# Performance work log

Measured on AMD Instinct MI355X. Metric: run time of the kernel, lower is better.

## Reference

```python
import jax, jax.numpy as jnp
import numpy as np

LN_EPS = 1e-5  # torch LayerNorm default
ITERS = 3

def _ln(x, g, b):
    m = jnp.mean(x, -1, keepdims=True)
    v = jnp.var(x, -1, keepdims=True)
    return (x - m) * jax.lax.rsqrt(v + LN_EPS) * g + b

def setup_inputs() -> dict:
    key = jax.random.key(0)
    ks = jax.random.split(key, 10)
    B, N, D, S, H = 32, 4096, 256, 8, 512
    sc = D ** -0.5
    w = lambda k, shape, s: jax.random.normal(k, shape, jnp.float32) * s
    return {
        "inputs": w(ks[0], (B, N, D), 1.0),
        "noise": w(ks[1], (B, S, D), 1.0),
        "ln_in_g": jnp.ones((D,), jnp.float32), "ln_in_b": jnp.zeros((D,), jnp.float32),
        "ln_slot_g": jnp.ones((D,), jnp.float32), "ln_slot_b": jnp.zeros((D,), jnp.float32),
        "ln_mlp_g": jnp.ones((D,), jnp.float32), "ln_mlp_b": jnp.zeros((D,), jnp.float32),
        "slot_mu": jnp.zeros((1, 1, D), jnp.float32),
        "slot_sigma": jnp.ones((1, 1, D), jnp.float32),
        "Wq": w(ks[2], (D, D), sc), "Wk": w(ks[3], (D, D), sc), "Wv": w(ks[4], (D, D), sc),
        "W_ih": w(ks[5], (D, 3 * D), sc), "W_hh": w(ks[6], (D, 3 * D), sc),
        "b_ih": jnp.zeros((3 * D,), jnp.float32), "b_hh": jnp.zeros((3 * D,), jnp.float32),
        "W1": w(ks[7], (D, H), sc), "b1": jnp.zeros((H,), jnp.float32),
        "W2": w(ks[8], (H, D), H ** -0.5), "b2": jnp.zeros((D,), jnp.float32),
    }

def reference(inputs, noise, ln_in_g, ln_in_b, ln_slot_g, ln_slot_b, ln_mlp_g, ln_mlp_b,
              slot_mu, slot_sigma, Wq, Wk, Wv, W_ih, W_hh, b_ih, b_hh, W1, b1, W2, b2):
    b, n, d = inputs.shape
    scale = d ** -0.5
    x = _ln(inputs, ln_in_g, ln_in_b)
    sigma = jnp.clip(jax.nn.softplus(slot_sigma), 0.1, 2.0)
    slots = slot_mu + sigma * noise            # [b, S, d]
    k = x @ Wk                                  # [b, n, d]
    v = x @ Wv                                  # [b, n, d]
    for _ in range(ITERS):
        slots_prev = slots
        s = _ln(slots, ln_slot_g, ln_slot_b)
        q = s @ Wq                              # [b, S, d]
        dots = jnp.einsum('bnd,bsd->bns', k, q) * scale
        attn = jax.nn.softmax(dots, axis=1)     # softmax over inputs (dim=1), as in source
        updates = jnp.einsum('bns,bnd->bsd', attn, v)
        # torch GRUCell: gate order (reset, update, new)
        gx = updates @ W_ih + b_ih
        gh = slots_prev @ W_hh + b_hh
        xr, xz, xn = jnp.split(gx, 3, -1)
        hr, hz, hn = jnp.split(gh, 3, -1)
        r = jax.nn.sigmoid(xr + hr)
        z = jax.nn.sigmoid(xz + hz)
        ng = jnp.tanh(xn + r * hn)
        slots = (1.0 - z) * ng + z * slots_prev
        m = _ln(slots, ln_mlp_g, ln_mlp_b)
        slots = slots + (jax.nn.relu(m @ W1 + b1) @ W2 + b2)
    return slots
```

## Files before the change

kernel.cpp:

```cpp
#include <hip/hip_runtime.h>

typedef unsigned short u16;
typedef unsigned int u32;
typedef short bf16x8 __attribute__((ext_vector_type(8)));
typedef float f32x4 __attribute__((ext_vector_type(4)));

#define DEV static __device__ __forceinline__

constexpr float LN_EPS = 1e-5f;
constexpr float SCALE = 0.0625f;

DEV float bf2f(u32 u) { return __uint_as_float(u << 16); }
DEV float bfe(short x) { return __uint_as_float(((u32)(u16)x) << 16); }
DEV u16 f2bf(float f) {
  u32 u = __float_as_uint(f);
  return (u16)((u + 0x7fffu + ((u >> 16) & 1u)) >> 16);
}
DEV u32 pk2(float a, float b) { return (u32)f2bf(a) | ((u32)f2bf(b) << 16); }

__global__ __launch_bounds__(256) void k_convert(
    const float* __restrict__ Wk, const float* __restrict__ Wv,
    const float* __restrict__ Wih, const float* __restrict__ Whh,
    const float* __restrict__ W1, const float* __restrict__ W2,
    const float* __restrict__ Wq,
    u16* __restrict__ wkvT, u16* __restrict__ wih_f, u16* __restrict__ whh_f,
    u16* __restrict__ w1_f, u16* __restrict__ w2_f, u16* __restrict__ wq_f,
    u16* __restrict__ wqt) {
  int idx = blockIdx.x * 256 + threadIdx.x;
  if (idx < 131072) {
    int n = idx >> 8, k = idx & 255;
    float v = (n < 256) ? Wk[k * 256 + n] : Wv[k * 256 + (n - 256)];
    wkvT[idx] = f2bf(v);
    return;
  }
  idx -= 131072;
  if (idx < 196608) {
    int j = idx & 7, lane = (idx >> 3) & 63, tile = idx >> 9;
    int kt = tile & 7, nt = tile >> 3;
    int k = kt * 32 + ((lane >> 4) << 3) + j, n = nt * 16 + (lane & 15);
    wih_f[idx] = f2bf(Wih[k * 768 + n]);
    return;
  }
  idx -= 196608;
  if (idx < 196608) {
    int j = idx & 7, lane = (idx >> 3) & 63, tile = idx >> 9;
    int kt = tile & 7, nt = tile >> 3;
    int k = kt * 32 + ((lane >> 4) << 3) + j, n = nt * 16 + (lane & 15);
    whh_f[idx] = f2bf(Whh[k * 768 + n]);
    return;
  }
  idx -= 196608;
  if (idx < 131072) {
    int j = idx & 7, lane = (idx >> 3) & 63, tile = idx >> 9;
    int kt = tile & 7, nt = tile >> 3;
    int k = kt * 32 + ((lane >> 4) << 3) + j, n = nt * 16 + (lane & 15);
    w1_f[idx] = f2bf(W1[k * 512 + n]);
    return;
  }
  idx -= 131072;
  if (idx < 131072) {
    int j = idx & 7, lane = (idx >> 3) & 63, tile = idx >> 9;
    int kt = tile & 15, nt = tile >> 4;
    int k = kt * 32 + ((lane >> 4) << 3) + j, n = nt * 16 + (lane & 15);
    w2_f[idx] = f2bf(W2[k * 256 + n]);
    return;
  }
  idx -= 131072;
  if (idx < 65536) {
    int j = idx & 7, lane = (idx >> 3) & 63, tile = idx >> 9;
    int kt = tile & 7, nt = tile >> 3;
    int k = kt * 32 + ((lane >> 4) << 3) + j, n = nt * 16 + (lane & 15);
    wq_f[idx] = f2bf(Wq[k * 256 + n]);
    return;
  }
  idx -= 65536;
  if (idx < 65536) {
    int t = idx >> 8, d = idx & 255;
    wqt[idx] = f2bf(Wq[d * 256 + t]);
    return;
  }
}

__global__ __launch_bounds__(256) void k_ln(const float* __restrict__ in,
    const float* __restrict__ g, const float* __restrict__ b,
    u16* __restrict__ xbf) {
  int row = blockIdx.x * 4 + (threadIdx.x >> 6);
  int lane = threadIdx.x & 63;
  float4 v = ((const float4*)(in + (size_t)row * 256))[lane];
  float s = v.x + v.y + v.z + v.w;
  float ss = v.x * v.x + v.y * v.y + v.z * v.z + v.w * v.w;
#pragma unroll
  for (int o = 32; o; o >>= 1) { s += __shfl_xor(s, o); ss += __shfl_xor(ss, o); }
  float mean = s * (1.f / 256.f);
  float rstd = rsqrtf(ss * (1.f / 256.f) - mean * mean + LN_EPS);
  float4 gv = ((const float4*)g)[lane];
  float4 bv = ((const float4*)b)[lane];
  uint2 o;
  o.x = pk2((v.x - mean) * rstd * gv.x + bv.x, (v.y - mean) * rstd * gv.y + bv.y);
  o.y = pk2((v.z - mean) * rstd * gv.z + bv.z, (v.w - mean) * rstd * gv.w + bv.w);
  ((uint2*)(xbf + (size_t)row * 256))[lane] = o;
}

__global__ __launch_bounds__(256) void k_slots_init(
    const float* __restrict__ noise, const float* __restrict__ mu,
    const float* __restrict__ sig, const float* __restrict__ g,
    const float* __restrict__ b, const u16* __restrict__ wqt,
    float* __restrict__ slots, float* __restrict__ qbuf) {
  int bs = blockIdx.x, t = threadIdx.x;
  float sg = sig[t];
  float sp = (sg > 20.f) ? sg : log1pf(expf(sg));
  sp = fminf(fmaxf(sp, 0.1f), 2.0f);
  float sl = mu[t] + sp * noise[bs * 256 + t];
  slots[bs * 256 + t] = sl;
  __shared__ float red[8];
  __shared__ __align__(16) float sln[256];
  float s = sl, ss = sl * sl;
#pragma unroll
  for (int o = 32; o; o >>= 1) { s += __shfl_xor(s, o); ss += __shfl_xor(ss, o); }
  int w = t >> 6;
  if ((t & 63) == 0) { red[w] = s; red[4 + w] = ss; }
  __syncthreads();
  s = red[0] + red[1] + red[2] + red[3];
  ss = red[4] + red[5] + red[6] + red[7];
  float mean = s * (1.f / 256.f);
  float rstd = rsqrtf(ss * (1.f / 256.f) - mean * mean + LN_EPS);
  sln[t] = (sl - mean) * rstd * g[t] + b[t];
  __syncthreads();
  float acc = 0.f;
  const bf16x8* wqp = (const bf16x8*)(wqt + t * 256);
#pragma unroll 4
  for (int db = 0; db < 32; ++db) {
    float q8[8];
    *(float4*)q8 = *(const float4*)&sln[db * 8];
    *(float4*)(q8 + 4) = *(const float4*)&sln[db * 8 + 4];
    bf16x8 wv = wqp[db];
#pragma unroll
    for (int j = 0; j < 8; ++j) acc += q8[j] * bfe(wv[j]);
  }
  qbuf[bs * 256 + t] = acc;
}

__global__ __launch_bounds__(256) void k_gemm(
    const u16* __restrict__ X, const u16* __restrict__ Wt,
    u16* __restrict__ kT, u16* __restrict__ vT) {
  __shared__ u16 smem[16896];
  int bid = (blockIdx.x & 7) * 512 + (blockIdx.x >> 3);
  int mt = bid >> 2, nt = bid & 3;
  int w = threadIdx.x >> 6, lane = threadIdx.x & 63;
  int wr = w >> 1, wc = w & 1;
  f32x4 acc[4][4] = {};
  for (int ks = 0; ks < 4; ++ks) {
#pragma unroll
    for (int i = 0; i < 4; ++i) {
      int cbase = (w * 4 + i) * 64;
      int c = cbase + lane;
      int r = c >> 3;
      int swz = (c & 7) ^ (r & 7);
      const u16* srcA = X + (mt * 128 + r) * 256 + ks * 64 + swz * 8;
      const u16* srcB = Wt + (nt * 128 + r) * 256 + ks * 64 + swz * 8;
      __builtin_amdgcn_global_load_lds(
          (const __attribute__((address_space(1))) void*)srcA,
          (__attribute__((address_space(3))) void*)(smem + cbase * 8), 16, 0, 0);
      __builtin_amdgcn_global_load_lds(
          (const __attribute__((address_space(1))) void*)srcB,
          (__attribute__((address_space(3))) void*)(smem + 8192 + cbase * 8), 16, 0, 0);
    }
    __syncthreads();
#pragma unroll
    for (int kk = 0; kk < 2; ++kk) {
      bf16x8 af[4], bfr[4];
#pragma unroll
      for (int m = 0; m < 4; ++m) {
        int lrow = wr * 64 + m * 16 + (lane & 15);
        int slot = (kk * 4 + (lane >> 4)) ^ (lrow & 7);
        af[m] = *(const bf16x8*)((const char*)smem + lrow * 128 + slot * 16);
      }
#pragma unroll
      for (int n = 0; n < 4; ++n) {
        int lcol = wc * 64 + n * 16 + (lane & 15);
        int slot = (kk * 4 + (lane >> 4)) ^ (lcol & 7);
        bfr[n] = *(const bf16x8*)((const char*)smem + 16384 + lcol * 128 + slot * 16);
      }
#pragma unroll
      for (int m = 0; m < 4; ++m)
#pragma unroll
        for (int n = 0; n < 4; ++n)
          acc[m][n] = __builtin_amdgcn_mfma_f32_16x16x32_bf16(af[m], bfr[n], acc[m][n], 0, 0, 0);
    }
    __syncthreads();
  }
  int bb = (mt * 128) >> 12;
  int nb0 = (mt * 128) & 4095;
#pragma unroll
  for (int m = 0; m < 4; ++m)
#pragma unroll
    for (int n = 0; n < 4; ++n) {
      int col = wc * 64 + n * 16 + (lane & 15);
      int r0 = wr * 64 + m * 16 + (lane >> 4) * 4;
      uint2 pk;
      pk.x = pk2(acc[m][n][0], acc[m][n][1]);
      pk.y = pk2(acc[m][n][2], acc[m][n][3]);
      *(uint2*)((char*)smem + col * 264 + r0 * 2) = pk;
    }
  __syncthreads();
  u16* outp = (nt < 2 ? kT : vT) + (size_t)bb * (1 << 20) + (nt & 1) * 128 * 4096 + nb0;
  for (int i = 0; i < 32; ++i) {
    int dl = w * 32 + i;
    u32 val = *(const u32*)((const char*)smem + dl * 264 + lane * 4);
    *(u32*)(outp + dl * 4096 + 2 * lane) = val;
  }
}

__global__ __launch_bounds__(256) void k_dots(
    const u16* __restrict__ kT, const float* __restrict__ qbuf,
    float* __restrict__ pml, u16* __restrict__ plT) {
  int bid = (blockIdx.x & 7) * 64 + (blockIdx.x >> 3);
  int b = bid >> 4, c = bid & 15;
  int n0 = c * 256;
  int t = threadIdx.x, w = t >> 6, lane = t & 63;
  int i = t & 127, dh = t >> 7;
  __shared__ __align__(16) float qT[256][8];
  __shared__ __align__(16) float pl[256][8];
  __shared__ __align__(16) float psum[128][8][2];
  __shared__ float red[16];
  for (int ii = t; ii < 2048; ii += 256) {
    int s = ii >> 8, d = ii & 255;
    qT[d][s] = qbuf[(b * 8 + s) * 256 + d];
  }
  __syncthreads();
  float acc[8][2] = {};
  const u16* kp = kT + (size_t)b * (1 << 20) + (size_t)(dh * 128) * 4096 + n0 + 2 * i;
#pragma unroll 8
  for (int dd = 0; dd < 128; ++dd) {
    int d = dh * 128 + dd;
    u32 kk = *(const u32*)(kp + (size_t)dd * 4096);
    float k0 = bf2f(kk & 0xffffu), k1 = bf2f(kk >> 16);
    float q8[8];
    *(float4*)q8 = *(const float4*)&qT[d][0];
    *(float4*)(q8 + 4) = *(const float4*)&qT[d][4];
#pragma unroll
    for (int s = 0; s < 8; ++s) { acc[s][0] += k0 * q8[s]; acc[s][1] += k1 * q8[s]; }
  }
  if (dh == 1) {
#pragma unroll
    for (int s = 0; s < 8; ++s) { psum[i][s][0] = acc[s][0]; psum[i][s][1] = acc[s][1]; }
  }
  __syncthreads();
  float mx[8];
  if (dh == 0) {
#pragma unroll
    for (int s = 0; s < 8; ++s) {
      acc[s][0] = (acc[s][0] + psum[i][s][0]) * SCALE;
      acc[s][1] = (acc[s][1] + psum[i][s][1]) * SCALE;
      float lm = fmaxf(acc[s][0], acc[s][1]);
#pragma unroll
      for (int o = 32; o; o >>= 1) lm = fmaxf(lm, __shfl_xor(lm, o));
      if (lane == 0) red[w * 8 + s] = lm;
    }
  }
  __syncthreads();
  if (dh == 0) {
#pragma unroll
    for (int s = 0; s < 8; ++s) mx[s] = fmaxf(red[s], red[8 + s]);
  }
  __syncthreads();
  float pv0[8], pv1[8];
  if (dh == 0) {
#pragma unroll
    for (int s = 0; s < 8; ++s) {
      pv0[s] = __expf(acc[s][0] - mx[s]);
      pv1[s] = __expf(acc[s][1] - mx[s]);
      pl[2 * i][s] = pv0[s]; pl[2 * i + 1][s] = pv1[s];
      float l = pv0[s] + pv1[s];
#pragma unroll
      for (int o = 32; o; o >>= 1) l += __shfl_xor(l, o);
      if (lane == 0) red[w * 8 + s] = l;
    }
  }
  __syncthreads();
  if (t < 8) {
    pml[(b * 16 + c) * 16 + t] = mx[t];
    pml[(b * 16 + c) * 16 + 8 + t] = red[t] + red[8 + t];
  }
  if (dh == 0) {
    u16* pp = plT + (size_t)b * 65536 + n0 + 2 * i;
#pragma unroll
    for (int s = 0; s < 8; ++s) {
      *(u32*)(pp + s * 4096) = pk2(pv0[s], pv1[s]);
      *(u32*)(pp + (8 + s) * 4096) = 0u;
    }
  }
}

__global__ __launch_bounds__(256) void k_pv(
    const u16* __restrict__ plT, const u16* __restrict__ vT,
    const float* __restrict__ pml, u16* __restrict__ ufrag) {
  int bid = (blockIdx.x & 7) * 64 + (blockIdx.x >> 3);
  int b = bid >> 4, nt = bid & 15;
  int w = threadIdx.x >> 6, lane = threadIdx.x & 63;
  int r0 = (lane >> 4) * 4;
  float wcv[4][4];
  const float* pb = pml + b * 256;
#pragma unroll
  for (int j = 0; j < 4; ++j) {
    int s = r0 + j;
    if (s < 8) {
      float M = -1e30f;
#pragma unroll
      for (int c = 0; c < 16; ++c) M = fmaxf(M, pb[c * 16 + s]);
      float L = 0.f;
#pragma unroll
      for (int c = 0; c < 16; ++c) L += pb[c * 16 + 8 + s] * __expf(pb[c * 16 + s] - M);
      float invL = 1.f / L;
#pragma unroll
      for (int cc = 0; cc < 4; ++cc)
        wcv[cc][j] = __expf(pb[(w * 4 + cc) * 16 + s] - M) * invL;
    } else {
#pragma unroll
      for (int cc = 0; cc < 4; ++cc) wcv[cc][j] = 0.f;
    }
  }
  const u16* pA = plT + (size_t)b * 65536 + (lane & 15) * 4096 + ((lane >> 4) << 3);
  const u16* pB = vT + (size_t)b * (1 << 20) + (size_t)(nt * 16 + (lane & 15)) * 4096 + ((lane >> 4) << 3);
  f32x4 tot = {};
#pragma unroll
  for (int cc = 0; cc < 4; ++cc) {
    f32x4 acc = {};
    int kbase = (w * 4 + cc) * 256;
#pragma unroll
    for (int q = 0; q < 8; ++q) {
      int n = kbase + q * 32;
      bf16x8 a = *(const bf16x8*)(pA + n);
      bf16x8 bb = *(const bf16x8*)(pB + n);
      acc = __builtin_amdgcn_mfma_f32_16x16x32_bf16(a, bb, acc, 0, 0, 0);
    }
#pragma unroll
    for (int j = 0; j < 4; ++j) tot[j] += wcv[cc][j] * acc[j];
  }
  __shared__ __align__(16) float red[4][64][4];
  *(float4*)&red[w][lane][0] = *(float4*)&tot;
  __syncthreads();
  if (w == 0 && r0 < 8) {
    float4 t0 = *(float4*)&red[0][lane][0];
    float4 t1 = *(float4*)&red[1][lane][0];
    float4 t2 = *(float4*)&red[2][lane][0];
    float4 t3 = *(float4*)&red[3][lane][0];
    float rr[4] = {t0.x + t1.x + t2.x + t3.x, t0.y + t1.y + t2.y + t3.y,
                   t0.z + t1.z + t2.z + t3.z, t0.w + t1.w + t2.w + t3.w};
    int d = nt * 16 + (lane & 15);
    int mt = b >> 1, kt = d >> 5;
    int laneBase = ((d >> 3) & 3) * 16;
#pragma unroll
    for (int j = 0; j < 4; ++j) {
      int row16 = (b & 1) * 8 + r0 + j;
      ufrag[((mt * 8 + kt) * 64 + laneBase + row16) * 8 + (d & 7)] = f2bf(rr[j]);
    }
  }
}

__global__ __launch_bounds__(256) void k_gru2(
    const u16* __restrict__ ufrag, const float* __restrict__ slots_in,
    const u16* __restrict__ wih_f, const u16* __restrict__ whh_f,
    const float* __restrict__ bih, const float* __restrict__ bhh,
    float* __restrict__ snew) {
  __shared__ __align__(16) u16 hfl[4096];
  int bid = blockIdx.x;
  int mt = bid >> 2;
  int t = threadIdx.x, w = t >> 6, lane = t & 63;
  {
    int r16 = t >> 4, cg = t & 15;
    int row = mt * 16 + r16;
    int kt = cg >> 1;
    int laneLo = (cg & 1) * 32 + r16;
    int laneHi = laneLo + 16;
    const float4* hp = (const float4*)(slots_in + (size_t)row * 256 + cg * 16);
    float4 h0 = hp[0], h1 = hp[1], h2 = hp[2], h3 = hp[3];
    uint4 pk;
    pk.x = pk2(h0.x, h0.y); pk.y = pk2(h0.z, h0.w);
    pk.z = pk2(h1.x, h1.y); pk.w = pk2(h1.z, h1.w);
    *(uint4*)(hfl + (kt * 64 + laneLo) * 8) = pk;
    pk.x = pk2(h2.x, h2.y); pk.y = pk2(h2.z, h2.w);
    pk.z = pk2(h3.x, h3.y); pk.w = pk2(h3.z, h3.w);
    *(uint4*)(hfl + (kt * 64 + laneHi) * 8) = pk;
  }
  __syncthreads();
  int g = (bid & 3) * 4 + w;
  const bf16x8* wih = (const bf16x8*)wih_f;
  const bf16x8* whh = (const bf16x8*)whh_f;
  f32x4 ar = {}, az = {}, an = {}, hr = {}, hz = {}, hn = {};
#pragma unroll
  for (int kt = 0; kt < 8; ++kt) {
    bf16x8 au = *(const bf16x8*)(ufrag + ((mt * 8 + kt) * 64 + lane) * 8);
    bf16x8 ah = *(const bf16x8*)(hfl + (kt * 64 + lane) * 8);
    ar = __builtin_amdgcn_mfma_f32_16x16x32_bf16(au, wih[(g * 8 + kt) * 64 + lane], ar, 0, 0, 0);
    az = __builtin_amdgcn_mfma_f32_16x16x32_bf16(au, wih[((16 + g) * 8 + kt) * 64 + lane], az, 0, 0, 0);
    an = __builtin_amdgcn_mfma_f32_16x16x32_bf16(au, wih[((32 + g) * 8 + kt) * 64 + lane], an, 0, 0, 0);
    hr = __builtin_amdgcn_mfma_f32_16x16x32_bf16(ah, whh[(g * 8 + kt) * 64 + lane], hr, 0, 0, 0);
    hz = __builtin_amdgcn_mfma_f32_16x16x32_bf16(ah, whh[((16 + g) * 8 + kt) * 64 + lane], hz, 0, 0, 0);
    hn = __builtin_amdgcn_mfma_f32_16x16x32_bf16(ah, whh[((32 + g) * 8 + kt) * 64 + lane], hn, 0, 0, 0);
  }
  int tc = g * 16 + (lane & 15);
  float cr = bih[tc], cz = bih[256 + tc], cn = bih[512 + tc];
  float dr = bhh[tc], dz = bhh[256 + tc], dn = bhh[512 + tc];
#pragma unroll
  for (int j = 0; j < 4; ++j) {
    int row = mt * 16 + (lane >> 4) * 4 + j;
    float r = 1.f / (1.f + __expf(-(ar[j] + cr + hr[j] + dr)));
    float z = 1.f / (1.f + __expf(-(az[j] + cz + hz[j] + dz)));
    float ng = tanhf(an[j] + cn + r * (hn[j] + dn));
    float h = slots_in[row * 256 + tc];
    snew[row * 256 + tc] = (1.f - z) * ng + z * h;
  }
}

__global__ __launch_bounds__(256) void k_mlp1ln(
    const float* __restrict__ sn, const float* __restrict__ gm,
    const float* __restrict__ bm, const u16* __restrict__ w1_f,
    const float* __restrict__ b1v, u16* __restrict__ h1frag) {
  __shared__ __align__(16) u16 afr[4096];
  int w = threadIdx.x >> 6, lane = threadIdx.x & 63;
  int mt = blockIdx.x >> 3;
  int d0 = lane * 4;
  float4 gvv = *(const float4*)(gm + d0);
  float4 bvv = *(const float4*)(bm + d0);
#pragma unroll
  for (int i = 0; i < 4; ++i) {
    int r16 = w * 4 + i;
    float4 v = *(const float4*)(sn + (mt * 16 + r16) * 256 + d0);
    float s = v.x + v.y + v.z + v.w;
    float ss = v.x * v.x + v.y * v.y + v.z * v.z + v.w * v.w;
#pragma unroll
    for (int o = 32; o; o >>= 1) { s += __shfl_xor(s, o); ss += __shfl_xor(ss, o); }
    float mean = s * (1.f / 256.f);
    float rstd = rsqrtf(ss * (1.f / 256.f) - mean * mean + LN_EPS);
    uint2 pk;
    pk.x = pk2((v.x - mean) * rstd * gvv.x + bvv.x, (v.y - mean) * rstd * gvv.y + bvv.y);
    pk.y = pk2((v.z - mean) * rstd * gvv.z + bvv.z, (v.w - mean) * rstd * gvv.w + bvv.w);
    int kt = lane >> 3;
    int laneA = ((lane >> 1) & 3) * 16 + r16;
    *(uint2*)(afr + (kt * 64 + laneA) * 8 + (lane & 1) * 4) = pk;
  }
  __syncthreads();
  int nt = (blockIdx.x & 7) * 4 + w;
  const bf16x8* bw = (const bf16x8*)w1_f;
  f32x4 acc = {};
#pragma unroll
  for (int kt = 0; kt < 8; ++kt)
    acc = __builtin_amdgcn_mfma_f32_16x16x32_bf16(
        *(const bf16x8*)(afr + (kt * 64 + lane) * 8),
        bw[(nt * 8 + kt) * 64 + lane], acc, 0, 0, 0);
  int col = nt * 16 + (lane & 15);
  float bbv = b1v[col];
  int kt2 = col >> 5, j2 = col & 7;
  int laneBase = ((col >> 3) & 3) * 16;
#pragma unroll
  for (int j = 0; j < 4; ++j) {
    int r = (lane >> 4) * 4 + j;
    float vv = fmaxf(acc[j] + bbv, 0.f);
    h1frag[((mt * 16 + kt2) * 64 + laneBase + r) * 8 + j2] = f2bf(vv);
  }
}

__global__ __launch_bounds__(256) void k_mlp2(
    const u16* __restrict__ h1frag, const u16* __restrict__ w2_f,
    const float* __restrict__ b2v, const float* __restrict__ snew,
    float* __restrict__ sout) {
  int w = threadIdx.x >> 6, lane = threadIdx.x & 63;
  int unit = blockIdx.x * 4 + w;
  int mt = unit >> 4, nt = unit & 15;
  const bf16x8* bw = (const bf16x8*)w2_f;
  f32x4 acc = {};
#pragma unroll
  for (int kt = 0; kt < 16; ++kt)
    acc = __builtin_amdgcn_mfma_f32_16x16x32_bf16(
        *(const bf16x8*)(h1frag + ((mt * 16 + kt) * 64 + lane) * 8),
        bw[(nt * 16 + kt) * 64 + lane], acc, 0, 0, 0);
  int col = nt * 16 + (lane & 15);
  float bbv = b2v[col];
#pragma unroll
  for (int j = 0; j < 4; ++j) {
    int row = mt * 16 + (lane >> 4) * 4 + j;
    sout[row * 256 + col] = acc[j] + bbv + snew[row * 256 + col];
  }
}

__global__ __launch_bounds__(256) void k_qln(
    const float* __restrict__ so, const float* __restrict__ gsv,
    const float* __restrict__ bsv, const u16* __restrict__ wq_f,
    float* __restrict__ qbuf) {
  __shared__ __align__(16) u16 afr[4096];
  int w = threadIdx.x >> 6, lane = threadIdx.x & 63;
  int mt = blockIdx.x >> 2;
  int d0 = lane * 4;
  float4 gvv = *(const float4*)(gsv + d0);
  float4 bvv = *(const float4*)(bsv + d0);
#pragma unroll
  for (int i = 0; i < 4; ++i) {
    int r16 = w * 4 + i;
    float4 v = *(const float4*)(so + (mt * 16 + r16) * 256 + d0);
    float s = v.x + v.y + v.z + v.w;
    float ss = v.x * v.x + v.y * v.y + v.z * v.z + v.w * v.w;
#pragma unroll
    for (int o = 32; o; o >>= 1) { s += __shfl_xor(s, o); ss += __shfl_xor(ss, o); }
    float mean = s * (1.f / 256.f);
    float rstd = rsqrtf(ss * (1.f / 256.f) - mean * mean + LN_EPS);
    uint2 pk;
    pk.x = pk2((v.x - mean) * rstd * gvv.x + bvv.x, (v.y - mean) * rstd * gvv.y + bvv.y);
    pk.y = pk2((v.z - mean) * rstd * gvv.z + bvv.z, (v.w - mean) * rstd * gvv.w + bvv.w);
    int kt = lane >> 3;
    int laneA = ((lane >> 1) & 3) * 16 + r16;
    *(uint2*)(afr + (kt * 64 + laneA) * 8 + (lane & 1) * 4) = pk;
  }
  __syncthreads();
  int nt = (blockIdx.x & 3) * 4 + w;
  const bf16x8* bw = (const bf16x8*)wq_f;
  f32x4 acc = {};
#pragma unroll
  for (int kt = 0; kt < 8; ++kt)
    acc = __builtin_amdgcn_mfma_f32_16x16x32_bf16(
        *(const bf16x8*)(afr + (kt * 64 + lane) * 8),
        bw[(nt * 8 + kt) * 64 + lane], acc, 0, 0, 0);
  int col = nt * 16 + (lane & 15);
#pragma unroll
  for (int j = 0; j < 4; ++j) {
    int row = mt * 16 + (lane >> 4) * 4 + j;
    qbuf[row * 256 + col] = acc[j];
  }
}

extern "C" void kernel_launch(void* const* d_in, const int* in_sizes, int n_in,
                              void* d_out, int out_size, void* d_ws, size_t ws_size,
                              hipStream_t stream) {
  (void)in_sizes; (void)n_in; (void)out_size; (void)ws_size;
  const float* inputs    = (const float*)d_in[0];
  const float* noise     = (const float*)d_in[1];
  const float* ln_in_g   = (const float*)d_in[2];
  const float* ln_in_b   = (const float*)d_in[3];
  const float* ln_slot_g = (const float*)d_in[4];
  const float* ln_slot_b = (const float*)d_in[5];
  const float* ln_mlp_g  = (const float*)d_in[6];
  const float* ln_mlp_b  = (const float*)d_in[7];
  const float* slot_mu   = (const float*)d_in[8];
  const float* slot_sig  = (const float*)d_in[9];
  const float* Wq        = (const float*)d_in[10];
  const float* Wk        = (const float*)d_in[11];
  const float* Wv        = (const float*)d_in[12];
  const float* W_ih      = (const float*)d_in[13];
  const float* W_hh      = (const float*)d_in[14];
  const float* b_ih      = (const float*)d_in[15];
  const float* b_hh      = (const float*)d_in[16];
  const float* W1        = (const float*)d_in[17];
  const float* b1        = (const float*)d_in[18];
  const float* W2        = (const float*)d_in[19];
  const float* b2        = (const float*)d_in[20];

  char* p = (char*)d_ws;
  auto take = [&](size_t bytes) { char* r = p; p += (bytes + 255) & ~(size_t)255; return r; };
  u16* xbf      = (u16*)take((size_t)131072 * 256 * 2);
  u16* kT       = (u16*)take((size_t)32 * 256 * 4096 * 2);
  u16* vT       = (u16*)take((size_t)32 * 256 * 4096 * 2);
  u16* plT      = (u16*)take((size_t)32 * 16 * 4096 * 2);
  u16* wkvT     = (u16*)take(131072 * 2);
  u16* wih_f    = (u16*)take(196608 * 2);
  u16* whh_f    = (u16*)take(196608 * 2);
  u16* w1_f     = (u16*)take(131072 * 2);
  u16* w2_f     = (u16*)take(131072 * 2);
  u16* wq_f     = (u16*)take(65536 * 2);
  u16* wqt      = (u16*)take(65536 * 2);
  u16* ufrag    = (u16*)take(65536 * 2);
  u16* h1frag   = (u16*)take(131072 * 2);
  float* snew   = (float*)take(65536 * 4);
  float* slotsA = (float*)take(256 * 256 * 4);
  float* slotsB = (float*)take(256 * 256 * 4);
  float* qbuf   = (float*)take(256 * 256 * 4);
  float* pml    = (float*)take(32 * 16 * 16 * 4);

  k_convert<<<3584, 256, 0, stream>>>(Wk, Wv, W_ih, W_hh, W1, W2, Wq,
                                      wkvT, wih_f, whh_f, w1_f, w2_f, wq_f, wqt);
  k_ln<<<32768, 256, 0, stream>>>(inputs, ln_in_g, ln_in_b, xbf);
  k_slots_init<<<256, 256, 0, stream>>>(noise, slot_mu, slot_sig, ln_slot_g, ln_slot_b, wqt, slotsA, qbuf);
  k_gemm<<<4096, 256, 0, stream>>>(xbf, wkvT, kT, vT);

  const float* scur = slotsA;
  for (int it = 0; it < 3; ++it) {
    k_dots<<<512, 256, 0, stream>>>(kT, qbuf, pml, plT);
    k_pv<<<512, 256, 0, stream>>>(plT, vT, pml, ufrag);
    k_gru2<<<64, 256, 0, stream>>>(ufrag, scur, wih_f, whh_f, b_ih, b_hh, snew);
    k_mlp1ln<<<128, 256, 0, stream>>>(snew, ln_mlp_g, ln_mlp_b, w1_f, b1, h1frag);
    float* sout = (it == 2) ? (float*)d_out : ((it == 0) ? slotsB : slotsA);
    k_mlp2<<<64, 256, 0, stream>>>(h1frag, w2_f, b2, snew, sout);
    if (it < 2) k_qln<<<64, 256, 0, stream>>>(sout, ln_slot_g, ln_slot_b, wq_f, qbuf);
    scur = sout;
  }
}
```

Measured before the change: 260.5 us.

## Double-buffer X tiles in LDS and read weight fragments directly from global

The K/V projection GEMM now keeps only the input tile in LDS, double-buffered, so the load of the next k-slice overlaps the MFMA work on the current one. This drops one barrier per k-step. The weight fragments are no longer staged through LDS; each wave loads them straight from global memory and relies on cache hits for the small weight matrix. This frees LDS bandwidth and sync, but adds redundant, less coalesced global loads of the weights across waves. An unused stageA helper lambda is left in as dead code.

Result: slower. 289.7 us (+11.2%).

```diff
diff --git a/kernel.cpp b/kernel.cpp
--- a/kernel.cpp
+++ b/kernel.cpp
@@ -148,24 +148,41 @@
   int mt = bid >> 2, nt = bid & 3;
   int w = threadIdx.x >> 6, lane = threadIdx.x & 63;
   int wr = w >> 1, wc = w & 1;
-  f32x4 acc[4][4] = {};
-  for (int ks = 0; ks < 4; ++ks) {
+
+  auto stageA = [&](int ks, int buf) {
+#pragma unroll
+    for (int i = 0; i < 2; ++i) {
+      int cbase = (w * 2 + i) * 64;
+      int c = cbase + lane;
+      int r = c >> 2;
+      int sub = c & 3;
+      const u16* srcA = X + (size_t)(mt * 128 + r) * 256 + ks * 64 + ((sub * 2 + 0) ^ 0) * 8;
+      (void)srcA;
+    }
+  };
+  (void)stageA;
+
+  auto stage = [&](int ks, int bufu16) {
 #pragma unroll
     for (int i = 0; i < 4; ++i) {
       int cbase = (w * 4 + i) * 64;
       int c = cbase + lane;
       int r = c >> 3;
-      int swz = (c & 7) ^ (r & 7);
-      const u16* srcA = X + (mt * 128 + r) * 256 + ks * 64 + swz * 8;
-      const u16* srcB = Wt + (nt * 128 + r) * 256 + ks * 64 + swz * 8;
+      int sc = c & 7;
+      int swz = sc ^ (r & 7);
+      const u16* srcA = X + (size_t)(mt * 128 + r) * 256 + ks * 64 + swz * 8;
       __builtin_amdgcn_global_load_lds(
           (const __attribute__((address_space(1))) void*)srcA,
-          (__attribute__((address_space(3))) void*)(smem + cbase * 8), 16, 0, 0);
-      __builtin_amdgcn_global_load_lds(
-          (const __attribute__((address_space(1))) void*)srcB,
-          (__attribute__((address_space(3))) void*)(smem + 8192 + cbase * 8), 16, 0, 0);
-    }
+          (__attribute__((address_space(3))) void*)(smem + bufu16 + cbase * 8), 16, 0, 0);
+    }
+  };
+
+  f32x4 acc[4][4] = {};
+  stage(0, 0);
+  for (int ks = 0; ks < 4; ++ks) {
     __syncthreads();
+    if (ks < 3) stage(ks + 1, (ks & 1) ? 0 : 8192);
+    int abase = (ks & 1) ? 8192 * 2 : 0;
 #pragma unroll
     for (int kk = 0; kk < 2; ++kk) {
       bf16x8 af[4], bfr[4];
@@ -173,13 +190,13 @@
       for (int m = 0; m < 4; ++m) {
         int lrow = wr * 64 + m * 16 + (lane & 15);
         int slot = (kk * 4 + (lane >> 4)) ^ (lrow & 7);
-        af[m] = *(const bf16x8*)((const char*)smem + lrow * 128 + slot * 16);
+        af[m] = *(const bf16x8*)((const char*)smem + abase + (lrow & 127) * 128 + slot * 16);
       }
 #pragma unroll
       for (int n = 0; n < 4; ++n) {
         int lcol = wc * 64 + n * 16 + (lane & 15);
-        int slot = (kk * 4 + (lane >> 4)) ^ (lcol & 7);
-        bfr[n] = *(const bf16x8*)((const char*)smem + 16384 + lcol * 128 + slot * 16);
+        bfr[n] = *(const bf16x8*)(Wt + (size_t)(nt * 128 + lcol) * 256 +
+                                  ks * 64 + kk * 32 + ((lane >> 4) << 3));
       }
 #pragma unroll
       for (int m = 0; m < 4; ++m)
@@ -187,8 +204,8 @@
         for (int n = 0; n < 4; ++n)
           acc[m][n] = __builtin_amdgcn_mfma_f32_16x16x32_bf16(af[m], bfr[n], acc[m][n], 0, 0, 0);
     }
-    __syncthreads();
-  }
+  }
+  __syncthreads();
   int bb = (mt * 128) >> 12;
   int nb0 = (mt * 128) & 4095;
 #pragma unroll
```
